# Performance work log

Measured on AMD Instinct MI355X. Metric: run time of the kernel, lower is better.

The kernel has to match this reference:

```python
import jax, jax.numpy as jnp
import numpy as np
from jax import lax

N_STATES = 4096
N_OBS = 512
SEQ_LEN = 8192


def setup_inputs() -> dict:
    key = jax.random.key(0)
    k1, k2, k3 = jax.random.split(key, 3)
    observations = jax.random.randint(k1, (SEQ_LEN,), 0, N_OBS, dtype=jnp.int32)
    # row-stochastic transition matrix (single action, as in TorchCHMMSensory)
    T = jax.random.uniform(k2, (N_STATES, N_STATES), dtype=jnp.float32) + 1e-10
    T = T / T.sum(axis=1, keepdims=True)
    Pi_x = jax.random.uniform(k3, (N_STATES,), dtype=jnp.float32) + 1e-10
    Pi_x = Pi_x / Pi_x.sum()
    return {"T": T, "Pi_x": Pi_x, "observations": observations, "n_observations": N_OBS}


def _forward_backward(T, Pi_x, observations, n_observations):
    """Scaled CHMM forward-backward. Clone-structured deterministic emission:
    state s emits observation s // n_clones, so emission is an indicator mask."""
    S = T.shape[0]
    n_clones = S // n_observations
    state_obs = jnp.arange(S, dtype=jnp.int32) // n_clones  # [S]
    mask = (state_obs[None, :] == observations[:, None]).astype(T.dtype)  # [L, S]

    # --- forward pass (scaled alphas) ---
    a0 = Pi_x * mask[0]
    c0 = a0.sum()
    a0 = a0 / c0

    def fwd_step(alpha, m):
        a = (alpha @ T) * m   # message passing + clone-block restriction
        c = a.sum()
        a = a / c
        return a, (a, c)

    _, (al, cs) = lax.scan(fwd_step, a0, mask[1:])
    alphas = jnp.concatenate([a0[None], al])          # [L, S]
    cs = jnp.concatenate([c0[None], cs])              # [L]
    log_lik = jnp.sum(jnp.log(cs))

    # --- backward pass (scaled betas) ---
    def bwd_step(beta, mc):
        m, c = mc
        b = (T @ (m * beta)) / c
        return b, b

    bL = jnp.ones((S,), dtype=T.dtype)
    _, betas_rev = lax.scan(bwd_step, bL, (mask[1:], cs[1:]), reverse=True)
    betas = jnp.concatenate([betas_rev, bL[None]])    # [L, S]

    gamma = alphas * betas
    gamma = gamma / gamma.sum(axis=1, keepdims=True)  # posteriors [L, S]
    return log_lik, gamma


def reference(T, Pi_x, observations, n_observations):
    return _forward_backward(T, Pi_x, observations, n_observations)
```

## Files before the change

kernel.cpp:

```cpp
#include <hip/hip_runtime.h>


#define NSTATES 4096
#define NBLK    8
#define LSEQ    8192
#define NSTEPS  8191
#define CHK     32
#define NCH     256
#define NGRP    16
#define GSZ     16
#define NFILL   512
#define FROWS   16

#define OFF_P   0u
#define OFF_G2  16384u
#define OFF_LLP 17408u
#define FLG_F1  17664u
#define FLG_F2  17920u
#define FLG_F3  17936u
#define MAGIC   0x5A17C0DEu

__device__ __forceinline__ float aload(float* p) {
    return __hip_atomic_load(p, __ATOMIC_RELAXED, __HIP_MEMORY_SCOPE_AGENT);
}
__device__ __forceinline__ void astore(float* p, float v) {
    __hip_atomic_store(p, v, __ATOMIC_RELAXED, __HIP_MEMORY_SCOPE_AGENT);
}
__device__ __forceinline__ unsigned aloadu(unsigned* p) {
    return __hip_atomic_load(p, __ATOMIC_RELAXED, __HIP_MEMORY_SCOPE_AGENT);
}
__device__ __forceinline__ void astoreu(unsigned* p, unsigned v) {
    __hip_atomic_store(p, v, __ATOMIC_RELAXED, __HIP_MEMORY_SCOPE_AGENT);
}
#define VMFENCE()  asm volatile("s_waitcnt vmcnt(0)" ::: "memory")
#define LDSFENCE() asm volatile("s_waitcnt lgkmcnt(0)" ::: "memory")

__device__ __forceinline__ int expof(float x) {
    return (int)((__float_as_uint(x) >> 23) & 0xff) - 127;
}

__global__ __launch_bounds__(256) void kFB(const float* __restrict__ T,
                                           const float* __restrict__ Pi,
                                           const int* __restrict__ obs,
                                           float* __restrict__ out,
                                           float* __restrict__ ws)
{
    __shared__ float sM[CHK * 64];
    __shared__ float sDuty[GSZ * 64];
    __shared__ float sG2[NGRP * 64];
    __shared__ float sGP[GSZ * 64];
    __shared__ float sA[(CHK + 1) * 8];
    __shared__ float sB[(CHK + 1) * 8];
    __shared__ float sGv[CHK * 8];
    __shared__ int   sObs[CHK + 1];
    unsigned* flg = reinterpret_cast<unsigned*>(ws);
    const int tid = threadIdx.x;
    const int blk = blockIdx.x;

    if (blk >= NCH) {
        const int f = blk - NCH;
        const int r0 = f * FROWS;
        if (tid < FROWS + 1) {
            int t = r0 - 1 + tid;
            sObs[tid] = (t >= 0) ? obs[t] : 0;
        }
        __syncthreads();
        float4* o4 = reinterpret_cast<float4*>(out);
        const float4 z = make_float4(0.f, 0.f, 0.f, 0.f);
        const int wv = tid >> 6, lane = tid & 63;
        int w2r[4];
#pragma unroll
        for (int k = 0; k < 4; ++k) w2r[k] = sObs[1 + wv * 4 + k] * 2;
#pragma unroll
        for (int k = 0; k < 4; ++k) {
            const int rr = wv * 4 + k;
            float4* rowp = o4 + (size_t)(r0 + rr) * 1024;
            const int w2 = w2r[k];
#pragma unroll
            for (int s = 0; s < 16; ++s) {
                int pos = s * 64 + lane;
                if (pos != 0 && (unsigned)(pos - w2) > 2u) rowp[pos] = z;
            }
        }
        if (tid < FROWS * 8) {
            const int rr = tid >> 3, role = tid & 7;
            const int r = r0 + rr;
            const int ob = sObs[1 + rr];
            const int obPrev = sObs[rr];
            const int m = r * 1024 + ob * 2;
            const int ks = r * 1024;
            const bool fullStraddle = (r != 0) && (obPrev != 511) && (ob != 0);
            if (role == 0) {
                if (fullStraddle) o4[ks] = z;
                else if (r != 0 && obPrev != 511) out[(size_t)4 * ks] = 0.f;
            } else if (role <= 3) {
                if (!fullStraddle && ob != 0) out[(size_t)4 * ks + role] = 0.f;
            } else if (role <= 6) {
                if (ob <= 510) out[(size_t)4 * m + 9 + (role - 4)] = 0.f;
            } else {
                if (ob >= 1) out[(size_t)4 * m] = 0.f;
            }
        }
        if (f == NFILL - 1 && tid == 255 && sObs[FROWS] != 511)
            out[(size_t)LSEQ * NSTATES] = 0.f;
        return;
    }

    if (tid >= 64) return;
    __builtin_amdgcn_s_setprio(1);
    const int b = blk;
    const int g = b >> 4, rIn = b & 15;
    const int t0 = b * CHK;
    const int n = min(CHK, NSTEPS - t0);
    float ll0 = 0.f;
    int kTot = 0;
    const int i = tid >> 3, j = tid & 7;

#pragma unroll
    for (int w = 0; w < 4; ++w) {
        int u = tid + 64 * w;
        int dt = u >> 3, ri = u & 7;
        if (dt < n) {
            int t = t0 + dt;
            int row = obs[t] * NBLK + ri;
            int col = obs[t + 1] * NBLK;
            const float4* src = reinterpret_cast<const float4*>(T + (size_t)row * NSTATES + col);
            float4 v0 = src[0], v1 = src[1];
            float vv[8] = {v0.x, v0.y, v0.z, v0.w, v1.x, v1.y, v1.z, v1.w};
            float* base = &sM[dt * 64 + ri];
#pragma unroll
            for (int jj = 0; jj < 8; ++jj) base[jj * 8] = vv[jj];
        }
    }
    if (tid < CHK) sObs[tid] = obs[t0 + tid];
    LDSFENCE();

    {
        float p = sM[j * 8 + i];
        float m[8], mn[8];
#pragma unroll
        for (int k = 0; k < 8; ++k) m[k] = sM[64 + j * 8 + k];
        for (int dt = 1; dt < n; ++dt) {
            int dtn = min(dt + 1, n - 1);
#pragma unroll
            for (int k = 0; k < 8; ++k) mn[k] = sM[dtn * 64 + j * 8 + k];
            float pn = 0.f;
#pragma unroll
            for (int k = 0; k < 8; ++k) pn = fmaf(__shfl(p, i * 8 + k, 64), m[k], pn);
            if ((dt & 3) == 0) {
                int ke = expof(__shfl(pn, 0, 64));
                pn = ldexpf(pn, -ke);
                kTot += ke;
            }
            p = pn;
#pragma unroll
            for (int k = 0; k < 8; ++k) m[k] = mn[k];
        }
        {
            int ke = expof(__shfl(p, 0, 64));
            p = ldexpf(p, -ke);
            kTot += ke;
        }
        astore(&ws[OFF_P + b * 64 + j * 8 + i], p);
    }
    VMFENCE();
    if (tid == 0) astoreu(&flg[FLG_F1 + b], MAGIC);

    if (b < NGRP) {
        for (;;) {
            bool ok = true;
            if (tid < GSZ)
                ok = aloadu(&flg[FLG_F1 + GSZ * b + tid]) == MAGIC;
            if (__all(ok)) break;
            __builtin_amdgcn_s_sleep(1);
        }
        {
            float rb[16];
#pragma unroll
            for (int k = 0; k < 16; ++k)
                rb[k] = aload(&ws[OFF_P + (size_t)b * GSZ * 64 + k * 64 + tid]);
#pragma unroll
            for (int k = 0; k < 16; ++k) sDuty[k * 64 + tid] = rb[k];
        }
        LDSFENCE();
        float p = sDuty[j * 8 + i];
        float m[8], mn[8];
#pragma unroll
        for (int k = 0; k < 8; ++k) m[k] = sDuty[64 + j * 8 + k];
        for (int r = 1; r < GSZ; ++r) {
            int rn = min(r + 1, GSZ - 1);
#pragma unroll
            for (int k = 0; k < 8; ++k) mn[k] = sDuty[rn * 64 + j * 8 + k];
            float pn = 0.f;
#pragma unroll
            for (int k = 0; k < 8; ++k) pn = fmaf(__shfl(p, i * 8 + k, 64), m[k], pn);
            if ((r & 1) == 0 || r == GSZ - 1) {
                int ke = expof(__shfl(pn, 0, 64));
                pn = ldexpf(pn, -ke);
            }
            p = pn;
#pragma unroll
            for (int k = 0; k < 8; ++k) m[k] = mn[k];
        }
        astore(&ws[OFF_G2 + b * 64 + j * 8 + i], p);
        VMFENCE();
        if (tid == 0) astoreu(&flg[FLG_F2 + b], MAGIC);
    }

    for (;;) {
        bool ok = true;
        if (tid < NGRP)
            ok = aloadu(&flg[FLG_F2 + tid]) == MAGIC;
        if (__all(ok)) break;
        __builtin_amdgcn_s_sleep(1);
    }
    {
        float ra[16], rb[16];
#pragma unroll
        for (int k = 0; k < 16; ++k) ra[k] = aload(&ws[OFF_G2 + k * 64 + tid]);
#pragma unroll
        for (int k = 0; k < 16; ++k)
            rb[k] = aload(&ws[OFF_P + (size_t)g * GSZ * 64 + k * 64 + tid]);
#pragma unroll
        for (int k = 0; k < 16; ++k) sG2[k * 64 + tid] = ra[k];
#pragma unroll
        for (int k = 0; k < 16; ++k) sGP[k * 64 + tid] = rb[k];
    }
    LDSFENCE();

    if (tid < 16) {
        const int grp = tid >> 3, l8 = tid & 7;
        const int st = grp ? 8 : 1;
        const int boff = grp ? l8 : l8 * 8;
        float v[8], vb[8];
        {
            float a = Pi[obs[0] * NBLK + l8];
            float s0 = a;
            s0 += __shfl_xor(s0, 1); s0 += __shfl_xor(s0, 2); s0 += __shfl_xor(s0, 4);
            float rs0 = 1.0f / s0;
#pragma unroll
            for (int q = 0; q < 8; ++q) v[q] = grp ? 0.125f : __shfl(a, q, 8) * rs0;
            ll0 = __logf(s0);
        }
        const int cap = grp ? (NGRP - 1 - g) : g;
        if (cap == 0) {
#pragma unroll
            for (int q = 0; q < 8; ++q) vb[q] = v[q];
        }
        {
            float m[8], mn[8];
            int gi0 = grp ? (NGRP - 1) : 0;
#pragma unroll
            for (int q = 0; q < 8; ++q) m[q] = sG2[gi0 * 64 + boff + q * st];
            for (int r = 0; r < NGRP - 1; ++r) {
                int rp = min(r + 1, NGRP - 2);
                int gin = grp ? (NGRP - 1 - rp) : rp;
#pragma unroll
                for (int q = 0; q < 8; ++q) mn[q] = sG2[gin * 64 + boff + q * st];
                float u = 0.f;
#pragma unroll
                for (int q = 0; q < 8; ++q) u = fmaf(v[q], m[q], u);
                float s = 0.f;
#pragma unroll
                for (int q = 0; q < 8; ++q) { float x = __shfl(u, q, 8); v[q] = x; s += x; }
                float rs = 1.0f / s;
#pragma unroll
                for (int q = 0; q < 8; ++q) v[q] *= rs;
                if (r + 1 == cap) {
#pragma unroll
                    for (int q = 0; q < 8; ++q) vb[q] = v[q];
                }
#pragma unroll
                for (int q = 0; q < 8; ++q) m[q] = mn[q];
            }
        }
#pragma unroll
        for (int q = 0; q < 8; ++q) v[q] = vb[q];
        const int cnt = grp ? (GSZ - 1 - rIn) : rIn;
        {
            float m[8], mn[8];
            int lc0 = grp ? (GSZ - 1) : 0;
#pragma unroll
            for (int k = 0; k < 8; ++k) m[k] = sGP[lc0 * 64 + boff + k * st];
            for (int q = 0; q < GSZ - 1; ++q) {
                bool act = q < cnt;
                int qn = q + 1 < cnt ? q + 1 : 0;
                int lcn = grp ? (GSZ - 1 - qn) : qn;
#pragma unroll
                for (int k = 0; k < 8; ++k) mn[k] = sGP[lcn * 64 + boff + k * st];
                float u = 0.f;
#pragma unroll
                for (int k = 0; k < 8; ++k) u = fmaf(v[k], m[k], u);
                float s = 0.f;
                float vn[8];
#pragma unroll
                for (int k = 0; k < 8; ++k) { float x = __shfl(u, k, 8); vn[k] = x; s += x; }
                float rs = 1.0f / s;
#pragma unroll
                for (int k = 0; k < 8; ++k) v[k] = act ? vn[k] * rs : v[k];
#pragma unroll
                for (int k = 0; k < 8; ++k) m[k] = mn[k];
            }
        }
        if (grp == 0) {
            float u = 0.f;
#pragma unroll
            for (int q2 = 0; q2 < 8; ++q2)
                u = fmaf(v[q2], sGP[rIn * 64 + l8 * 8 + q2], u);
            float ssum = u;
            ssum += __shfl_xor(ssum, 1); ssum += __shfl_xor(ssum, 2); ssum += __shfl_xor(ssum, 4);
            if (l8 == 0)
                astore(&ws[OFF_LLP + b], __logf(ssum) + (float)kTot * 0.69314718055994531f);
        }
        float* hist = grp ? sB : sA;
        hist[(grp ? n : 0) * 8 + l8] = v[l8];
        int mt0 = grp ? (n - 1) : 0;
        float m[8], mn[8];
#pragma unroll
        for (int q = 0; q < 8; ++q) m[q] = sM[mt0 * 64 + boff + q * st];
        for (int rr = 0; rr < n; ++rr) {
            int rn2 = min(rr + 1, n - 1);
            int mtn = grp ? (n - 1 - rn2) : rn2;
#pragma unroll
            for (int q = 0; q < 8; ++q) mn[q] = sM[mtn * 64 + boff + q * st];
            float u = 0.f;
#pragma unroll
            for (int q = 0; q < 8; ++q) u = fmaf(v[q], m[q], u);
            float s = 0.f;
#pragma unroll
            for (int q = 0; q < 8; ++q) { float x = __shfl(u, q, 8); v[q] = x; s += x; }
            float rs = 1.0f / s;
#pragma unroll
            for (int q = 0; q < 8; ++q) v[q] *= rs;
            hist[(grp ? (n - 1 - rr) : (rr + 1)) * 8 + l8] = v[l8];
#pragma unroll
            for (int q = 0; q < 8; ++q) m[q] = mn[q];
        }
    }
    LDSFENCE();

    {
        const int r0l = tid >> 3, ii = tid & 7;
#pragma unroll
        for (int k = 0; k < 4; ++k) {
            int rr = r0l + k * 8;
            float gp = sA[rr * 8 + ii] * sB[rr * 8 + ii];
            float gs = gp;
            gs += __shfl_xor(gs, 1); gs += __shfl_xor(gs, 2); gs += __shfl_xor(gs, 4);
            sGv[rr * 8 + ii] = gp / gs;
        }
    }
    LDSFENCE();
    VMFENCE();
    if (tid == 0) astoreu(&flg[FLG_F3 + b], MAGIC);
    __builtin_amdgcn_s_setprio(0);

    if (tid < CHK) {
        const int r = t0 + tid;
        const int ob = sObs[tid];
        const size_t W = (size_t)r * NSTATES + ob * NBLK;
        const float* gv = &sGv[tid * 8];
        out[W + 1] = gv[0];
        out[W + 2] = gv[1];
        out[W + 3] = gv[2];
        reinterpret_cast<float4*>(out)[W / 4 + 1] = make_float4(gv[3], gv[4], gv[5], gv[6]);
        out[W + 8] = gv[7];
    }

    if (b == 0) {
        for (;;) {
            bool ok = true;
#pragma unroll
            for (int q = 0; q < 4; ++q)
                ok = ok && (aloadu(&flg[FLG_F3 + tid * 4 + q]) == MAGIC);
            if (__all(ok)) break;
            __builtin_amdgcn_s_sleep(1);
        }
        float part = 0.f;
#pragma unroll
        for (int q = 0; q < 4; ++q) part += aload(&ws[OFF_LLP + tid * 4 + q]);
        part += __shfl_xor(part, 32); part += __shfl_xor(part, 16);
        part += __shfl_xor(part, 8);  part += __shfl_xor(part, 4);
        part += __shfl_xor(part, 2);  part += __shfl_xor(part, 1);
        if (tid == 0) out[0] = part + ll0;
    }
}

extern "C" void kernel_launch(void* const* d_in, const int* in_sizes, int n_in,
                              void* d_out, int out_size, void* d_ws, size_t ws_size,
                              hipStream_t stream)
{
    const float* T   = (const float*)d_in[0];
    const float* Pi  = (const float*)d_in[1];
    const int*   obs = (const int*)d_in[2];
    float* out = (float*)d_out;
    float* ws  = (float*)d_ws;

    kFB<<<NCH + NFILL, 256, 0, stream>>>(T, Pi, obs, out, ws);
}
```

Measured before the change: 41.60 us.

## Route gamma values through workspace so fill blocks write whole rows

Chain blocks now store their normalized posterior values into a workspace area instead of writing them into the output directly. Fill blocks zero their entire row range with plain contiguous float4 stores, with no per-observation masking. They then spin on the chain block's completion flag and write the eight nonzero gamma values into place. This removes the obs-dependent branching in the zero fill and the scattered writes from the latency-critical chain blocks. In exchange it adds a cross-block dependency: fill blocks must wait for chain blocks and may overwrite zeros, which depends on store ordering and on all blocks being co-resident.

```diff
diff --git a/kernel.cpp b/kernel.cpp
--- a/kernel.cpp
+++ b/kernel.cpp
@@ -15,6 +15,7 @@
 #define OFF_P   0u
 #define OFF_G2  16384u
 #define OFF_LLP 17408u
+#define OFF_G   18432u
 #define FLG_F1  17664u
 #define FLG_F2  17920u
 #define FLG_F3  17936u
@@ -51,8 +52,6 @@
     __shared__ float sGP[GSZ * 64];
     __shared__ float sA[(CHK + 1) * 8];
     __shared__ float sB[(CHK + 1) * 8];
-    __shared__ float sGv[CHK * 8];
-    __shared__ int   sObs[CHK + 1];
     unsigned* flg = reinterpret_cast<unsigned*>(ws);
     const int tid = threadIdx.x;
     const int blk = blockIdx.x;
@@ -60,49 +59,27 @@
     if (blk >= NCH) {
         const int f = blk - NCH;
         const int r0 = f * FROWS;
-        if (tid < FROWS + 1) {
-            int t = r0 - 1 + tid;
-            sObs[tid] = (t >= 0) ? obs[t] : 0;
-        }
-        __syncthreads();
+        if (tid < 3) out[1 + (size_t)r0 * 4096 + tid] = 0.f;
+        if (tid == 3) out[(size_t)(r0 + FROWS) * 4096] = 0.f;
         float4* o4 = reinterpret_cast<float4*>(out);
         const float4 z = make_float4(0.f, 0.f, 0.f, 0.f);
-        const int wv = tid >> 6, lane = tid & 63;
-        int w2r[4];
-#pragma unroll
-        for (int k = 0; k < 4; ++k) w2r[k] = sObs[1 + wv * 4 + k] * 2;
-#pragma unroll
-        for (int k = 0; k < 4; ++k) {
-            const int rr = wv * 4 + k;
-            float4* rowp = o4 + (size_t)(r0 + rr) * 1024;
-            const int w2 = w2r[k];
-#pragma unroll
-            for (int s = 0; s < 16; ++s) {
-                int pos = s * 64 + lane;
-                if (pos != 0 && (unsigned)(pos - w2) > 2u) rowp[pos] = z;
-            }
-        }
+        const size_t base = (size_t)r0 * 1024 + 1;
+#pragma unroll 8
+        for (int idx = tid; idx < FROWS * 1024 - 1; idx += 256)
+            o4[base + idx] = z;
+        __syncthreads();
+        if (tid == 0) {
+            while (aloadu(&flg[FLG_F3 + (f >> 1)]) != MAGIC)
+                __builtin_amdgcn_s_sleep(8);
+        }
+        __syncthreads();
         if (tid < FROWS * 8) {
-            const int rr = tid >> 3, role = tid & 7;
+            const int rr = tid >> 3, ii = tid & 7;
             const int r = r0 + rr;
-            const int ob = sObs[1 + rr];
-            const int obPrev = sObs[rr];
-            const int m = r * 1024 + ob * 2;
-            const int ks = r * 1024;
-            const bool fullStraddle = (r != 0) && (obPrev != 511) && (ob != 0);
-            if (role == 0) {
-                if (fullStraddle) o4[ks] = z;
-                else if (r != 0 && obPrev != 511) out[(size_t)4 * ks] = 0.f;
-            } else if (role <= 3) {
-                if (!fullStraddle && ob != 0) out[(size_t)4 * ks + role] = 0.f;
-            } else if (role <= 6) {
-                if (ob <= 510) out[(size_t)4 * m + 9 + (role - 4)] = 0.f;
-            } else {
-                if (ob >= 1) out[(size_t)4 * m] = 0.f;
-            }
-        }
-        if (f == NFILL - 1 && tid == 255 && sObs[FROWS] != 511)
-            out[(size_t)LSEQ * NSTATES] = 0.f;
+            const int ob = obs[r];
+            float gv = aload(&ws[OFF_G + (size_t)r * 8 + ii]);
+            out[1 + (size_t)r * 4096 + ob * NBLK + ii] = gv;
+        }
         return;
     }
 
@@ -132,7 +109,6 @@
             for (int jj = 0; jj < 8; ++jj) base[jj * 8] = vv[jj];
         }
     }
-    if (tid < CHK) sObs[tid] = obs[t0 + tid];
     LDSFENCE();
 
     {
@@ -347,25 +323,12 @@
             float gp = sA[rr * 8 + ii] * sB[rr * 8 + ii];
             float gs = gp;
             gs += __shfl_xor(gs, 1); gs += __shfl_xor(gs, 2); gs += __shfl_xor(gs, 4);
-            sGv[rr * 8 + ii] = gp / gs;
-        }
-    }
-    LDSFENCE();
+            astore(&ws[OFF_G + (size_t)(t0 + rr) * 8 + ii], gp / gs);
+        }
+    }
     VMFENCE();
     if (tid == 0) astoreu(&flg[FLG_F3 + b], MAGIC);
     __builtin_amdgcn_s_setprio(0);
-
-    if (tid < CHK) {
-        const int r = t0 + tid;
-        const int ob = sObs[tid];
-        const size_t W = (size_t)r * NSTATES + ob * NBLK;
-        const float* gv = &sGv[tid * 8];
-        out[W + 1] = gv[0];
-        out[W + 2] = gv[1];
-        out[W + 3] = gv[2];
-        reinterpret_cast<float4*>(out)[W / 4 + 1] = make_float4(gv[3], gv[4], gv[5], gv[6]);
-        out[W + 8] = gv[7];
-    }
 
     if (b == 0) {
         for (;;) {
```

New measurement: 42.15 us. Within noise of the previous version (+1.3%).
